# Kernel tuning notes

Hardware: AMD Instinct MI355X
Metric: run time of the kernel (lower is better)

The kernel has to match this reference:

```python
import jax, jax.numpy as jnp
import numpy as np

B = 100        # number of queries
N = 50000      # n_node
E = 600000     # n_edges
D = 128        # in_dim = out_dim (hidden_dim)
A = 64         # attn_dim
R = 200        # n_rel -> rela_embed has 2*R+1 = 401 rows


def setup_inputs() -> dict:
    key = jax.random.key(0)
    ks = jax.random.split(key, 14)
    q_sub = jax.random.randint(ks[0], (B,), 0, N)
    q_rel = jax.random.randint(ks[1], (B,), 0, 2 * R + 1)
    # edges: [E, 6]; col0=r_idx(<B), col2=rel(<2R+1), col4=sub(<N), col5=obj(<N); cols 1,3 unused
    c0 = jax.random.randint(ks[2], (E,), 0, B)
    c2 = jax.random.randint(ks[3], (E,), 0, 2 * R + 1)
    c4 = jax.random.randint(ks[4], (E,), 0, N)
    c5 = jax.random.randint(ks[5], (E,), 0, N)
    z = jnp.zeros((E,), dtype=jnp.int32)
    edges = jnp.stack([c0, z, c2, z, c4, c5], axis=1)
    hidden = jax.random.normal(ks[6], (N, D), dtype=jnp.float32)
    # learned parameters
    rela_embed = jax.random.normal(ks[7], (2 * R + 1, D), dtype=jnp.float32) * 0.02
    Ws = jax.random.normal(ks[8], (D, A), dtype=jnp.float32) * 0.05   # Ws_attn.weight^T
    Wr = jax.random.normal(ks[9], (D, A), dtype=jnp.float32) * 0.05   # Wr_attn.weight^T
    Wqr = jax.random.normal(ks[10], (D, A), dtype=jnp.float32) * 0.05 # Wqr_attn.weight^T
    bqr = jnp.zeros((A,), dtype=jnp.float32)
    wa = jax.random.normal(ks[11], (A, 1), dtype=jnp.float32) * 0.05  # w_alpha.weight^T
    ba = jnp.zeros((1,), dtype=jnp.float32)
    Wh = jax.random.normal(ks[12], (D, D), dtype=jnp.float32) * 0.05  # W_h.weight^T
    return {"q_sub": q_sub, "q_rel": q_rel, "hidden": hidden, "edges": edges,
            "n_node": N, "rela_embed": rela_embed, "Ws": Ws, "Wr": Wr,
            "Wqr": Wqr, "bqr": bqr, "wa": wa, "ba": ba, "Wh": Wh}


def reference(q_sub, q_rel, hidden, edges, n_node, rela_embed, Ws, Wr, Wqr, bqr, wa, ba, Wh):
    sub = edges[:, 4]
    rel = edges[:, 2]
    obj = edges[:, 5]
    r_idx = edges[:, 0]
    hs = hidden[sub]                       # [E, D] gather
    hr = rela_embed[rel]                   # [E, D] gather
    h_qr = rela_embed[q_rel][r_idx]        # [B, D] then gather -> [E, D]
    # attention score per edge
    pre = hs @ Ws + hr @ Wr + h_qr @ Wqr + bqr          # [E, A]
    alpha = jax.nn.sigmoid(jax.nn.relu(pre) @ wa + ba)   # [E, 1]
    message = alpha * (hs + hr)                          # [E, D]
    message_agg = jax.ops.segment_sum(message, obj, num_segments=n_node)  # [N, D]
    hidden_new = message_agg @ Wh                        # act = identity ('idd')
    return hidden_new
```

## Files before the change

### kernel.cpp

```cpp
#include <hip/hip_runtime.h>

#define DD 128
#define AA 64

static inline int idiv_up(int a, int b) { return (a + b - 1) / b; }

__global__ void rowmm_kernel(const float* __restrict__ src,
                             const float* __restrict__ W,
                             const float* __restrict__ bias,
                             const int* __restrict__ idx,
                             float* __restrict__ out, int nrows) {
    __shared__ float lds[4][DD];
    const int t = threadIdx.x;
    const int rl = t >> 6;
    const int a = t & 63;
    const int i = blockIdx.x * 4 + rl;
    if (i < nrows) {
        const int row = idx ? idx[i] : i;
        const float* srow = src + (long)row * DD;
        lds[rl][a]      = srow[a];
        lds[rl][a + 64] = srow[a + 64];
    }
    __syncthreads();
    if (i >= nrows) return;
    float acc = bias ? bias[a] : 0.0f;
    #pragma unroll 8
    for (int d = 0; d < DD; ++d)
        acc = fmaf(lds[rl][d], W[d * AA + a], acc);
    out[(long)i * AA + a] = acc;
}

__global__ void proj_gemm_kernel(const float* __restrict__ src,
                                 const float* __restrict__ W,
                                 float* __restrict__ out, int nrows) {
    __shared__ float lw[128 * 64];
    __shared__ float lht[128 * 64];
    const int t = threadIdx.x;
    const int rbase = blockIdx.x * 64;
    #pragma unroll
    for (int k = 0; k < 8192; k += 1024)
        *(float4*)&lw[k + t * 4] = *(const float4*)&W[k + t * 4];
    const int row = t & 63;
    const int d0 = (t >> 6) * 32;
    const int gr = rbase + row;
    #pragma unroll
    for (int j = 0; j < 8; ++j) {
        float4 v = make_float4(0.f, 0.f, 0.f, 0.f);
        if (gr < nrows) v = *(const float4*)&src[(long)gr * 128 + d0 + j * 4];
        lht[(d0 + j * 4 + 0) * 64 + row] = v.x;
        lht[(d0 + j * 4 + 1) * 64 + row] = v.y;
        lht[(d0 + j * 4 + 2) * 64 + row] = v.z;
        lht[(d0 + j * 4 + 3) * 64 + row] = v.w;
    }
    __syncthreads();
    const int r0 = (t & 15) * 4;
    const int c0 = (t >> 4) * 4;
    float acc[4][4] = {};
    #pragma unroll 4
    for (int d = 0; d < 128; ++d) {
        const float4 hv = *(const float4*)&lht[d * 64 + r0];
        const float4 wv = *(const float4*)&lw[d * 64 + c0];
        acc[0][0] = fmaf(hv.x, wv.x, acc[0][0]);
        acc[0][1] = fmaf(hv.x, wv.y, acc[0][1]);
        acc[0][2] = fmaf(hv.x, wv.z, acc[0][2]);
        acc[0][3] = fmaf(hv.x, wv.w, acc[0][3]);
        acc[1][0] = fmaf(hv.y, wv.x, acc[1][0]);
        acc[1][1] = fmaf(hv.y, wv.y, acc[1][1]);
        acc[1][2] = fmaf(hv.y, wv.z, acc[1][2]);
        acc[1][3] = fmaf(hv.y, wv.w, acc[1][3]);
        acc[2][0] = fmaf(hv.z, wv.x, acc[2][0]);
        acc[2][1] = fmaf(hv.z, wv.y, acc[2][1]);
        acc[2][2] = fmaf(hv.z, wv.z, acc[2][2]);
        acc[2][3] = fmaf(hv.z, wv.w, acc[2][3]);
        acc[3][0] = fmaf(hv.w, wv.x, acc[3][0]);
        acc[3][1] = fmaf(hv.w, wv.y, acc[3][1]);
        acc[3][2] = fmaf(hv.w, wv.z, acc[3][2]);
        acc[3][3] = fmaf(hv.w, wv.w, acc[3][3]);
    }
    #pragma unroll
    for (int i = 0; i < 4; ++i) {
        const int orow = rbase + r0 + i;
        if (orow < nrows)
            *(float4*)&out[(long)orow * 64 + c0] =
                make_float4(acc[i][0], acc[i][1], acc[i][2], acc[i][3]);
    }
}

__global__ void hist_kernel(const int* __restrict__ edges, int* deg, int E) {
    const int e = blockIdx.x * blockDim.x + threadIdx.x;
    if (e < E) atomicAdd(&deg[edges[(long)e * 6 + 5]], 1);
}

__global__ void scan1_kernel(const int* __restrict__ in, int* __restrict__ out,
                             int* __restrict__ bsum, int n) {
    __shared__ int tsum[256];
    const int t = threadIdx.x;
    const int base = blockIdx.x * 1024 + t * 4;
    int v[4];
    int s = 0;
    #pragma unroll
    for (int j = 0; j < 4; ++j) {
        v[j] = (base + j < n) ? in[base + j] : 0;
        s += v[j];
    }
    tsum[t] = s;
    __syncthreads();
    for (int o = 1; o < 256; o <<= 1) {
        int x = (t >= o) ? tsum[t - o] : 0;
        __syncthreads();
        tsum[t] += x;
        __syncthreads();
    }
    int run = (t > 0) ? tsum[t - 1] : 0;
    if (t == 255 && bsum) bsum[blockIdx.x] = tsum[255];
    #pragma unroll
    for (int j = 0; j < 4; ++j) {
        if (base + j < n) out[base + j] = run;
        run += v[j];
    }
}

__global__ void scan_add_kernel(int* offs, int* cur, const int* __restrict__ bsumx, int n) {
    const int i = blockIdx.x * blockDim.x + threadIdx.x;
    if (i < n) {
        const int v = offs[i] + bsumx[i >> 10];
        offs[i] = v;
        cur[i] = v;
    }
}

__global__ void scatter_kernel(const int* __restrict__ edges, int* cur,
                               int2* __restrict__ recs, int E) {
    const int e = blockIdx.x * blockDim.x + threadIdx.x;
    if (e >= E) return;
    const int* ed = edges + (long)e * 6;
    const int pos = atomicAdd(&cur[ed[5]], 1);
    recs[pos] = make_int2(ed[4], ed[2] | (ed[0] << 16));
}

__global__ void gather_kernel(const int2* __restrict__ recs,
                              const int* __restrict__ offs,
                              const float* __restrict__ hsWs,
                              const float* __restrict__ hrWr,
                              const float* __restrict__ hqrWqr,
                              const float* __restrict__ hidden,
                              const float* __restrict__ rela,
                              const float* __restrict__ wa,
                              const float* __restrict__ ba,
                              float* __restrict__ agg, int N, int E) {
    const int lane = threadIdx.x & 63;
    const int g = lane >> 4;
    const int l = lane & 15;
    const int v = (int)((blockIdx.x * blockDim.x + threadIdx.x) >> 6);
    if (v >= N) return;
    const float4 wav = *(const float4*)&wa[l * 4];
    const float bar = ba[0];
    const int start = offs[v];
    const int end = (v + 1 < N) ? offs[v + 1] : E;

    float4 acc0 = make_float4(0.f, 0.f, 0.f, 0.f);
    float4 acc1 = make_float4(0.f, 0.f, 0.f, 0.f);

    for (int base = start; base < end; base += 4) {
        const int k = base + g;
        const bool valid = (k < end);
        const int2 rec = valid ? recs[k] : make_int2(0, 0);
        const int sub  = rec.x;
        const int rel  = rec.y & 0xffff;
        const int ridx = rec.y >> 16;

        const float4 a4 = *(const float4*)&hsWs[sub * AA + l * 4];
        const float4 b4 = *(const float4*)&hrWr[rel * AA + l * 4];
        const float4 c4 = *(const float4*)&hqrWqr[ridx * AA + l * 4];
        float s = fmaxf(a4.x + b4.x + c4.x, 0.f) * wav.x;
        s = fmaf(fmaxf(a4.y + b4.y + c4.y, 0.f), wav.y, s);
        s = fmaf(fmaxf(a4.z + b4.z + c4.z, 0.f), wav.z, s);
        s = fmaf(fmaxf(a4.w + b4.w + c4.w, 0.f), wav.w, s);
        s += __shfl_xor(s, 1);
        s += __shfl_xor(s, 2);
        s += __shfl_xor(s, 4);
        s += __shfl_xor(s, 8);
        float alpha = __builtin_amdgcn_rcpf(1.0f + __expf(-(s + bar)));
        if (!valid) alpha = 0.0f;

        const float4 h0 = *(const float4*)&hidden[(long)sub * DD + l * 8];
        const float4 h1 = *(const float4*)&hidden[(long)sub * DD + l * 8 + 4];
        const float4 r0 = *(const float4*)&rela[rel * DD + l * 8];
        const float4 r1 = *(const float4*)&rela[rel * DD + l * 8 + 4];
        acc0.x = fmaf(alpha, h0.x + r0.x, acc0.x);
        acc0.y = fmaf(alpha, h0.y + r0.y, acc0.y);
        acc0.z = fmaf(alpha, h0.z + r0.z, acc0.z);
        acc0.w = fmaf(alpha, h0.w + r0.w, acc0.w);
        acc1.x = fmaf(alpha, h1.x + r1.x, acc1.x);
        acc1.y = fmaf(alpha, h1.y + r1.y, acc1.y);
        acc1.z = fmaf(alpha, h1.z + r1.z, acc1.z);
        acc1.w = fmaf(alpha, h1.w + r1.w, acc1.w);
    }

    #pragma unroll
    for (int o = 16; o <= 32; o <<= 1) {
        acc0.x += __shfl_xor(acc0.x, o);
        acc0.y += __shfl_xor(acc0.y, o);
        acc0.z += __shfl_xor(acc0.z, o);
        acc0.w += __shfl_xor(acc0.w, o);
        acc1.x += __shfl_xor(acc1.x, o);
        acc1.y += __shfl_xor(acc1.y, o);
        acc1.z += __shfl_xor(acc1.z, o);
        acc1.w += __shfl_xor(acc1.w, o);
    }
    if (g == 0) {
        *(float4*)&agg[(long)v * DD + l * 8]     = acc0;
        *(float4*)&agg[(long)v * DD + l * 8 + 4] = acc1;
    }
}

__global__ void out_gemm_kernel(const float* agg,
                                const float* __restrict__ Wh,
                                float* out, int nrows) {
    __shared__ float whs[64 * 128];
    __shared__ float ags[64 * 64];
    const int t = threadIdx.x;
    const int rbase = blockIdx.x * 64;
    const int j0 = (t & 31) * 4;
    const int rh = t >> 5;
    const int r0 = rh * 8;
    float acc[8][4];
    #pragma unroll
    for (int r = 0; r < 8; ++r)
        #pragma unroll
        for (int j = 0; j < 4; ++j) acc[r][j] = 0.0f;

    for (int dc = 0; dc < 128; dc += 64) {
        #pragma unroll
        for (int k = 0; k < 8192; k += 1024) {
            const int f = k + t * 4;
            *(float4*)&whs[f] = *(const float4*)&Wh[(long)dc * 128 + f];
        }
        #pragma unroll
        for (int k = 0; k < 4096; k += 1024) {
            const int f = k + t * 4;
            const int r = f >> 6;
            const int c = f & 63;
            float4 v = make_float4(0.0f, 0.0f, 0.0f, 0.0f);
            if (rbase + r < nrows)
                v = *(const float4*)&agg[(long)(rbase + r) * 128 + dc + c];
            *(float4*)&ags[f] = v;
        }
        __syncthreads();
        for (int d = 0; d < 64; d += 4) {
            const float4 wv0 = *(const float4*)&whs[(d + 0) * 128 + j0];
            const float4 wv1 = *(const float4*)&whs[(d + 1) * 128 + j0];
            const float4 wv2 = *(const float4*)&whs[(d + 2) * 128 + j0];
            const float4 wv3 = *(const float4*)&whs[(d + 3) * 128 + j0];
            #pragma unroll
            for (int r = 0; r < 8; ++r) {
                const float4 av = *(const float4*)&ags[(r0 + r) * 64 + d];
                acc[r][0] = fmaf(av.x, wv0.x, acc[r][0]);
                acc[r][1] = fmaf(av.x, wv0.y, acc[r][1]);
                acc[r][2] = fmaf(av.x, wv0.z, acc[r][2]);
                acc[r][3] = fmaf(av.x, wv0.w, acc[r][3]);
                acc[r][0] = fmaf(av.y, wv1.x, acc[r][0]);
                acc[r][1] = fmaf(av.y, wv1.y, acc[r][1]);
                acc[r][2] = fmaf(av.y, wv1.z, acc[r][2]);
                acc[r][3] = fmaf(av.y, wv1.w, acc[r][3]);
                acc[r][0] = fmaf(av.z, wv2.x, acc[r][0]);
                acc[r][1] = fmaf(av.z, wv2.y, acc[r][1]);
                acc[r][2] = fmaf(av.z, wv2.z, acc[r][2]);
                acc[r][3] = fmaf(av.z, wv2.w, acc[r][3]);
                acc[r][0] = fmaf(av.w, wv3.x, acc[r][0]);
                acc[r][1] = fmaf(av.w, wv3.y, acc[r][1]);
                acc[r][2] = fmaf(av.w, wv3.z, acc[r][2]);
                acc[r][3] = fmaf(av.w, wv3.w, acc[r][3]);
            }
        }
        __syncthreads();
    }
    #pragma unroll
    for (int r = 0; r < 8; ++r) {
        const int row = rbase + r0 + r;
        if (row < nrows)
            *(float4*)&out[(long)row * 128 + j0] =
                make_float4(acc[r][0], acc[r][1], acc[r][2], acc[r][3]);
    }
}

extern "C" void kernel_launch(void* const* d_in, const int* in_sizes, int n_in,
                              void* d_out, int out_size, void* d_ws, size_t ws_size,
                              hipStream_t stream) {
    const int*   q_rel  = (const int*)d_in[1];
    const float* hidden = (const float*)d_in[2];
    const int*   edges  = (const int*)d_in[3];
    const float* rela   = (const float*)d_in[5];
    const float* Ws     = (const float*)d_in[6];
    const float* Wr     = (const float*)d_in[7];
    const float* Wqr    = (const float*)d_in[8];
    const float* bqr    = (const float*)d_in[9];
    const float* wa     = (const float*)d_in[10];
    const float* ba     = (const float*)d_in[11];
    const float* Wh     = (const float*)d_in[12];

    const int B  = in_sizes[1];
    const int N  = in_sizes[2] / DD;
    const int E  = in_sizes[3] / 6;
    const int NR = in_sizes[5] / DD;

    float* out = (float*)d_out;

    float* hsWs   = (float*)d_ws;
    float* hrWr   = hsWs   + (size_t)N  * AA;
    float* hqrWqr = hrWr   + (size_t)NR * AA;
    int*   deg    = (int*)(hqrWqr + (size_t)B * AA);
    int*   cur    = deg  + N;
    int*   offs   = cur  + N;
    int*   bsum   = offs + N;
    int*   bsumx  = bsum + 64;
    int2*  recs   = (int2*)(bsumx + 64);

    const int nb = idiv_up(N, 1024);

    hipMemsetAsync(deg, 0, (size_t)N * sizeof(int), stream);
    proj_gemm_kernel<<<idiv_up(N, 64), 256, 0, stream>>>(hidden, Ws, hsWs, N);
    rowmm_kernel<<<idiv_up(NR, 4), 256, 0, stream>>>(rela, Wr, nullptr, nullptr, hrWr, NR);
    rowmm_kernel<<<idiv_up(B, 4), 256, 0, stream>>>(rela, Wqr, bqr, q_rel, hqrWqr, B);
    hist_kernel<<<idiv_up(E, 256), 256, 0, stream>>>(edges, deg, E);
    scan1_kernel<<<nb, 256, 0, stream>>>(deg, offs, bsum, N);
    scan1_kernel<<<1, 256, 0, stream>>>(bsum, bsumx, nullptr, nb);
    scan_add_kernel<<<idiv_up(N, 256), 256, 0, stream>>>(offs, cur, bsumx, N);
    scatter_kernel<<<idiv_up(E, 256), 256, 0, stream>>>(edges, cur, recs, E);
    gather_kernel<<<idiv_up(N * 64, 256), 256, 0, stream>>>(recs, offs, hsWs, hrWr, hqrWqr,
                                                            hidden, rela, wa, ba, out, N, E);
    out_gemm_kernel<<<idiv_up(N, 64), 256, 0, stream>>>(out, Wh, out, N);
}
```

Before: 306.1 us.

## Apply Wh before aggregation, merge projections into one kernel, store hsWs as bf16

Uses linearity to project hidden and rela_embed by Wh before the segment sum, so the gather accumulates already-transformed rows and the final out_gemm pass is dropped. All per-node and per-relation projections (Ws, Wr, Wqr, Wh) now run in one fused kernel launch. The hsWs attention term is stored as bf16 to halve its gather traffic. The trade-offs are an extra N×128 float intermediate written in the projection pass and reduced precision in the attention pre-activation.

After: 281.1 us. 1.09x faster.

```diff
diff --git a/kernel.cpp b/kernel.cpp
--- a/kernel.cpp
+++ b/kernel.cpp
@@ -5,84 +5,131 @@
 
 static inline int idiv_up(int a, int b) { return (a + b - 1) / b; }
 
-__global__ void rowmm_kernel(const float* __restrict__ src,
-                             const float* __restrict__ W,
-                             const float* __restrict__ bias,
-                             const int* __restrict__ idx,
-                             float* __restrict__ out, int nrows) {
-    __shared__ float lds[4][DD];
+__device__ __forceinline__ unsigned short f2bf(float f) {
+    unsigned u = __float_as_uint(f);
+    u += 0x7fff + ((u >> 16) & 1);
+    return (unsigned short)(u >> 16);
+}
+__device__ __forceinline__ float bf2f(unsigned short h) {
+    return __uint_as_float(((unsigned)h) << 16);
+}
+
+__global__ __launch_bounds__(256)
+void proj_all_kernel(const float* __restrict__ hidden,
+                     const float* __restrict__ rela,
+                     const int* __restrict__ q_rel,
+                     const float* __restrict__ Ws,
+                     const float* __restrict__ Wr,
+                     const float* __restrict__ Wqr,
+                     const float* __restrict__ bqr,
+                     const float* __restrict__ Wh,
+                     unsigned short* __restrict__ hsWs16,
+                     float* __restrict__ hiddenWh,
+                     float* __restrict__ hrWr,
+                     float* __restrict__ relaWh,
+                     float* __restrict__ hqrWqr,
+                     int N, int NR, int B, int nA, int nB) {
+    __shared__ float lht[128 * 64];
+    __shared__ float wbuf[128 * 64];
     const int t = threadIdx.x;
-    const int rl = t >> 6;
-    const int a = t & 63;
-    const int i = blockIdx.x * 4 + rl;
-    if (i < nrows) {
-        const int row = idx ? idx[i] : i;
-        const float* srow = src + (long)row * DD;
-        lds[rl][a]      = srow[a];
-        lds[rl][a + 64] = srow[a + 64];
-    }
-    __syncthreads();
-    if (i >= nrows) return;
-    float acc = bias ? bias[a] : 0.0f;
-    #pragma unroll 8
-    for (int d = 0; d < DD; ++d)
-        acc = fmaf(lds[rl][d], W[d * AA + a], acc);
-    out[(long)i * AA + a] = acc;
-}
-
-__global__ void proj_gemm_kernel(const float* __restrict__ src,
-                                 const float* __restrict__ W,
-                                 float* __restrict__ out, int nrows) {
-    __shared__ float lw[128 * 64];
-    __shared__ float lht[128 * 64];
-    const int t = threadIdx.x;
-    const int rbase = blockIdx.x * 64;
-    #pragma unroll
-    for (int k = 0; k < 8192; k += 1024)
-        *(float4*)&lw[k + t * 4] = *(const float4*)&W[k + t * 4];
+    const int bid = blockIdx.x;
+    int type, rbase, nrows;
+    const float* src;
+    if (bid < nA)           { type = 0; rbase = bid * 64;             nrows = N;  src = hidden; }
+    else if (bid < nA + nB) { type = 1; rbase = (bid - nA) * 64;      nrows = NR; src = rela; }
+    else                    { type = 2; rbase = (bid - nA - nB) * 64; nrows = B;  src = rela; }
+
     const int row = t & 63;
     const int d0 = (t >> 6) * 32;
     const int gr = rbase + row;
+    const float* srow = nullptr;
+    if (gr < nrows) {
+        const int sr = (type == 2) ? q_rel[gr] : gr;
+        srow = src + (long)sr * DD;
+    }
     #pragma unroll
     for (int j = 0; j < 8; ++j) {
         float4 v = make_float4(0.f, 0.f, 0.f, 0.f);
-        if (gr < nrows) v = *(const float4*)&src[(long)gr * 128 + d0 + j * 4];
+        if (srow) v = *(const float4*)&srow[d0 + j * 4];
         lht[(d0 + j * 4 + 0) * 64 + row] = v.x;
         lht[(d0 + j * 4 + 1) * 64 + row] = v.y;
         lht[(d0 + j * 4 + 2) * 64 + row] = v.z;
         lht[(d0 + j * 4 + 3) * 64 + row] = v.w;
     }
-    __syncthreads();
+
     const int r0 = (t & 15) * 4;
     const int c0 = (t >> 4) * 4;
-    float acc[4][4] = {};
-    #pragma unroll 4
-    for (int d = 0; d < 128; ++d) {
-        const float4 hv = *(const float4*)&lht[d * 64 + r0];
-        const float4 wv = *(const float4*)&lw[d * 64 + c0];
-        acc[0][0] = fmaf(hv.x, wv.x, acc[0][0]);
-        acc[0][1] = fmaf(hv.x, wv.y, acc[0][1]);
-        acc[0][2] = fmaf(hv.x, wv.z, acc[0][2]);
-        acc[0][3] = fmaf(hv.x, wv.w, acc[0][3]);
-        acc[1][0] = fmaf(hv.y, wv.x, acc[1][0]);
-        acc[1][1] = fmaf(hv.y, wv.y, acc[1][1]);
-        acc[1][2] = fmaf(hv.y, wv.z, acc[1][2]);
-        acc[1][3] = fmaf(hv.y, wv.w, acc[1][3]);
-        acc[2][0] = fmaf(hv.z, wv.x, acc[2][0]);
-        acc[2][1] = fmaf(hv.z, wv.y, acc[2][1]);
-        acc[2][2] = fmaf(hv.z, wv.z, acc[2][2]);
-        acc[2][3] = fmaf(hv.z, wv.w, acc[2][3]);
-        acc[3][0] = fmaf(hv.w, wv.x, acc[3][0]);
-        acc[3][1] = fmaf(hv.w, wv.y, acc[3][1]);
-        acc[3][2] = fmaf(hv.w, wv.z, acc[3][2]);
-        acc[3][3] = fmaf(hv.w, wv.w, acc[3][3]);
-    }
-    #pragma unroll
-    for (int i = 0; i < 4; ++i) {
-        const int orow = rbase + r0 + i;
-        if (orow < nrows)
-            *(float4*)&out[(long)orow * 64 + c0] =
-                make_float4(acc[i][0], acc[i][1], acc[i][2], acc[i][3]);
+    const int nph = (type == 2) ? 1 : 3;
+
+    for (int p = 0; p < nph; ++p) {
+        const float* W;
+        int ldw, off;
+        if (p == 0) {
+            W = (type == 0) ? Ws : (type == 1) ? Wr : Wqr;
+            ldw = 64; off = 0;
+        } else {
+            W = Wh; ldw = 128; off = (p - 1) * 64;
+        }
+        #pragma unroll
+        for (int k = 0; k < 8192; k += 1024) {
+            const int f = k + t * 4;
+            *(float4*)&wbuf[f] = *(const float4*)&W[(long)(f >> 6) * ldw + off + (f & 63)];
+        }
+        __syncthreads();
+
+        float acc[4][4] = {};
+        #pragma unroll 4
+        for (int d = 0; d < 128; ++d) {
+            const float4 hv = *(const float4*)&lht[d * 64 + r0];
+            const float4 wv = *(const float4*)&wbuf[d * 64 + c0];
+            acc[0][0] = fmaf(hv.x, wv.x, acc[0][0]);
+            acc[0][1] = fmaf(hv.x, wv.y, acc[0][1]);
+            acc[0][2] = fmaf(hv.x, wv.z, acc[0][2]);
+            acc[0][3] = fmaf(hv.x, wv.w, acc[0][3]);
+            acc[1][0] = fmaf(hv.y, wv.x, acc[1][0]);
+            acc[1][1] = fmaf(hv.y, wv.y, acc[1][1]);
+            acc[1][2] = fmaf(hv.y, wv.z, acc[1][2]);
+            acc[1][3] = fmaf(hv.y, wv.w, acc[1][3]);
+            acc[2][0] = fmaf(hv.z, wv.x, acc[2][0]);
+            acc[2][1] = fmaf(hv.z, wv.y, acc[2][1]);
+            acc[2][2] = fmaf(hv.z, wv.z, acc[2][2]);
+            acc[2][3] = fmaf(hv.z, wv.w, acc[2][3]);
+            acc[3][0] = fmaf(hv.w, wv.x, acc[3][0]);
+            acc[3][1] = fmaf(hv.w, wv.y, acc[3][1]);
+            acc[3][2] = fmaf(hv.w, wv.z, acc[3][2]);
+            acc[3][3] = fmaf(hv.w, wv.w, acc[3][3]);
+        }
+
+        #pragma unroll
+        for (int i = 0; i < 4; ++i) {
+            const int orow = rbase + r0 + i;
+            if (orow >= nrows) continue;
+            if (type == 0) {
+                if (p == 0) {
+                    ushort4 o;
+                    o.x = f2bf(acc[i][0]); o.y = f2bf(acc[i][1]);
+                    o.z = f2bf(acc[i][2]); o.w = f2bf(acc[i][3]);
+                    *(ushort4*)&hsWs16[(long)orow * 64 + c0] = o;
+                } else {
+                    *(float4*)&hiddenWh[(long)orow * 128 + off + c0] =
+                        make_float4(acc[i][0], acc[i][1], acc[i][2], acc[i][3]);
+                }
+            } else if (type == 1) {
+                if (p == 0) {
+                    *(float4*)&hrWr[(long)orow * 64 + c0] =
+                        make_float4(acc[i][0], acc[i][1], acc[i][2], acc[i][3]);
+                } else {
+                    *(float4*)&relaWh[(long)orow * 128 + off + c0] =
+                        make_float4(acc[i][0], acc[i][1], acc[i][2], acc[i][3]);
+                }
+            } else {
+                const float4 bq = *(const float4*)&bqr[c0];
+                *(float4*)&hqrWqr[(long)orow * 64 + c0] =
+                    make_float4(acc[i][0] + bq.x, acc[i][1] + bq.y,
+                                acc[i][2] + bq.z, acc[i][3] + bq.w);
+            }
+        }
+        __syncthreads();
     }
 }
 
@@ -138,16 +185,17 @@
     recs[pos] = make_int2(ed[4], ed[2] | (ed[0] << 16));
 }
 
-__global__ void gather_kernel(const int2* __restrict__ recs,
-                              const int* __restrict__ offs,
-                              const float* __restrict__ hsWs,
-                              const float* __restrict__ hrWr,
-                              const float* __restrict__ hqrWqr,
-                              const float* __restrict__ hidden,
-                              const float* __restrict__ rela,
-                              const float* __restrict__ wa,
-                              const float* __restrict__ ba,
-                              float* __restrict__ agg, int N, int E) {
+__global__ __launch_bounds__(256)
+void gather_kernel(const int2* __restrict__ recs,
+                   const int* __restrict__ offs,
+                   const unsigned short* __restrict__ hsWs16,
+                   const float* __restrict__ hrWr,
+                   const float* __restrict__ hqrWqr,
+                   const float* __restrict__ hiddenWh,
+                   const float* __restrict__ relaWh,
+                   const float* __restrict__ wa,
+                   const float* __restrict__ ba,
+                   float* __restrict__ out, int N, int E) {
     const int lane = threadIdx.x & 63;
     const int g = lane >> 4;
     const int l = lane & 15;
@@ -169,13 +217,13 @@
         const int rel  = rec.y & 0xffff;
         const int ridx = rec.y >> 16;
 
-        const float4 a4 = *(const float4*)&hsWs[sub * AA + l * 4];
+        const ushort4 hw = *(const ushort4*)&hsWs16[(long)sub * AA + l * 4];
         const float4 b4 = *(const float4*)&hrWr[rel * AA + l * 4];
         const float4 c4 = *(const float4*)&hqrWqr[ridx * AA + l * 4];
-        float s = fmaxf(a4.x + b4.x + c4.x, 0.f) * wav.x;
-        s = fmaf(fmaxf(a4.y + b4.y + c4.y, 0.f), wav.y, s);
-        s = fmaf(fmaxf(a4.z + b4.z + c4.z, 0.f), wav.z, s);
-        s = fmaf(fmaxf(a4.w + b4.w + c4.w, 0.f), wav.w, s);
+        float s = fmaxf(bf2f(hw.x) + b4.x + c4.x, 0.f) * wav.x;
+        s = fmaf(fmaxf(bf2f(hw.y) + b4.y + c4.y, 0.f), wav.y, s);
+        s = fmaf(fmaxf(bf2f(hw.z) + b4.z + c4.z, 0.f), wav.z, s);
+        s = fmaf(fmaxf(bf2f(hw.w) + b4.w + c4.w, 0.f), wav.w, s);
         s += __shfl_xor(s, 1);
         s += __shfl_xor(s, 2);
         s += __shfl_xor(s, 4);
@@ -183,10 +231,10 @@
         float alpha = __builtin_amdgcn_rcpf(1.0f + __expf(-(s + bar)));
         if (!valid) alpha = 0.0f;
 
-        const float4 h0 = *(const float4*)&hidden[(long)sub * DD + l * 8];
-        const float4 h1 = *(const float4*)&hidden[(long)sub * DD + l * 8 + 4];
-        const float4 r0 = *(const float4*)&rela[rel * DD + l * 8];
-        const float4 r1 = *(const float4*)&rela[rel * DD + l * 8 + 4];
+        const float4 h0 = *(const float4*)&hiddenWh[(long)sub * DD + l * 8];
+        const float4 h1 = *(const float4*)&hiddenWh[(long)sub * DD + l * 8 + 4];
+        const float4 r0 = *(const float4*)&relaWh[rel * DD + l * 8];
+        const float4 r1 = *(const float4*)&relaWh[rel * DD + l * 8 + 4];
         acc0.x = fmaf(alpha, h0.x + r0.x, acc0.x);
         acc0.y = fmaf(alpha, h0.y + r0.y, acc0.y);
         acc0.z = fmaf(alpha, h0.z + r0.z, acc0.z);
@@ -209,78 +257,8 @@
         acc1.w += __shfl_xor(acc1.w, o);
     }
     if (g == 0) {
-        *(float4*)&agg[(long)v * DD + l * 8]     = acc0;
-        *(float4*)&agg[(long)v * DD + l * 8 + 4] = acc1;
-    }
-}
-
-__global__ void out_gemm_kernel(const float* agg,
-                                const float* __restrict__ Wh,
-                                float* out, int nrows) {
-    __shared__ float whs[64 * 128];
-    __shared__ float ags[64 * 64];
-    const int t = threadIdx.x;
-    const int rbase = blockIdx.x * 64;
-    const int j0 = (t & 31) * 4;
-    const int rh = t >> 5;
-    const int r0 = rh * 8;
-    float acc[8][4];
-    #pragma unroll
-    for (int r = 0; r < 8; ++r)
-        #pragma unroll
-        for (int j = 0; j < 4; ++j) acc[r][j] = 0.0f;
-
-    for (int dc = 0; dc < 128; dc += 64) {
-        #pragma unroll
-        for (int k = 0; k < 8192; k += 1024) {
-            const int f = k + t * 4;
-            *(float4*)&whs[f] = *(const float4*)&Wh[(long)dc * 128 + f];
-        }
-        #pragma unroll
-        for (int k = 0; k < 4096; k += 1024) {
-            const int f = k + t * 4;
-            const int r = f >> 6;
-            const int c = f & 63;
-            float4 v = make_float4(0.0f, 0.0f, 0.0f, 0.0f);
-            if (rbase + r < nrows)
-                v = *(const float4*)&agg[(long)(rbase + r) * 128 + dc + c];
-            *(float4*)&ags[f] = v;
-        }
-        __syncthreads();
-        for (int d = 0; d < 64; d += 4) {
-            const float4 wv0 = *(const float4*)&whs[(d + 0) * 128 + j0];
-            const float4 wv1 = *(const float4*)&whs[(d + 1) * 128 + j0];
-            const float4 wv2 = *(const float4*)&whs[(d + 2) * 128 + j0];
-            const float4 wv3 = *(const float4*)&whs[(d + 3) * 128 + j0];
-            #pragma unroll
-            for (int r = 0; r < 8; ++r) {
-                const float4 av = *(const float4*)&ags[(r0 + r) * 64 + d];
-                acc[r][0] = fmaf(av.x, wv0.x, acc[r][0]);
-                acc[r][1] = fmaf(av.x, wv0.y, acc[r][1]);
-                acc[r][2] = fmaf(av.x, wv0.z, acc[r][2]);
-                acc[r][3] = fmaf(av.x, wv0.w, acc[r][3]);
-                acc[r][0] = fmaf(av.y, wv1.x, acc[r][0]);
-                acc[r][1] = fmaf(av.y, wv1.y, acc[r][1]);
-                acc[r][2] = fmaf(av.y, wv1.z, acc[r][2]);
-                acc[r][3] = fmaf(av.y, wv1.w, acc[r][3]);
-                acc[r][0] = fmaf(av.z, wv2.x, acc[r][0]);
-                acc[r][1] = fmaf(av.z, wv2.y, acc[r][1]);
-                acc[r][2] = fmaf(av.z, wv2.z, acc[r][2]);
-                acc[r][3] = fmaf(av.z, wv2.w, acc[r][3]);
-                acc[r][0] = fmaf(av.w, wv3.x, acc[r][0]);
-                acc[r][1] = fmaf(av.w, wv3.y, acc[r][1]);
-                acc[r][2] = fmaf(av.w, wv3.z, acc[r][2]);
-                acc[r][3] = fmaf(av.w, wv3.w, acc[r][3]);
-            }
-        }
-        __syncthreads();
-    }
-    #pragma unroll
-    for (int r = 0; r < 8; ++r) {
-        const int row = rbase + r0 + r;
-        if (row < nrows)
-            *(float4*)&out[(long)row * 128 + j0] =
-                make_float4(acc[r][0], acc[r][1], acc[r][2], acc[r][3]);
+        *(float4*)&out[(long)v * DD + l * 8]     = acc0;
+        *(float4*)&out[(long)v * DD + l * 8 + 4] = acc1;
     }
 }
 
@@ -306,28 +284,32 @@
 
     float* out = (float*)d_out;
 
-    float* hsWs   = (float*)d_ws;
-    float* hrWr   = hsWs   + (size_t)N  * AA;
-    float* hqrWqr = hrWr   + (size_t)NR * AA;
-    int*   deg    = (int*)(hqrWqr + (size_t)B * AA);
-    int*   cur    = deg  + N;
-    int*   offs   = cur  + N;
-    int*   bsum   = offs + N;
-    int*   bsumx  = bsum + 64;
-    int2*  recs   = (int2*)(bsumx + 64);
-
+    unsigned short* hsWs16 = (unsigned short*)d_ws;
+    float* hiddenWh = (float*)(hsWs16 + (size_t)N * AA);
+    float* hrWr     = hiddenWh + (size_t)N * DD;
+    float* relaWh   = hrWr + (size_t)NR * AA;
+    float* hqrWqr   = relaWh + (size_t)NR * DD;
+    int*   deg      = (int*)(hqrWqr + (size_t)B * AA);
+    int*   cur      = deg  + N;
+    int*   offs     = cur  + N;
+    int*   bsum     = offs + N;
+    int*   bsumx    = bsum + 64;
+    int2*  recs     = (int2*)(bsumx + 64);
+
+    const int nA = idiv_up(N, 64);
+    const int nB = idiv_up(NR, 64);
+    const int nC = idiv_up(B, 64);
     const int nb = idiv_up(N, 1024);
 
     hipMemsetAsync(deg, 0, (size_t)N * sizeof(int), stream);
-    proj_gemm_kernel<<<idiv_up(N, 64), 256, 0, stream>>>(hidden, Ws, hsWs, N);
-    rowmm_kernel<<<idiv_up(NR, 4), 256, 0, stream>>>(rela, Wr, nullptr, nullptr, hrWr, NR);
-    rowmm_kernel<<<idiv_up(B, 4), 256, 0, stream>>>(rela, Wqr, bqr, q_rel, hqrWqr, B);
+    proj_all_kernel<<<nA + nB + nC, 256, 0, stream>>>(
+        hidden, rela, q_rel, Ws, Wr, Wqr, bqr, Wh,
+        hsWs16, hiddenWh, hrWr, relaWh, hqrWqr, N, NR, B, nA, nB);
     hist_kernel<<<idiv_up(E, 256), 256, 0, stream>>>(edges, deg, E);
     scan1_kernel<<<nb, 256, 0, stream>>>(deg, offs, bsum, N);
     scan1_kernel<<<1, 256, 0, stream>>>(bsum, bsumx, nullptr, nb);
     scan_add_kernel<<<idiv_up(N, 256), 256, 0, stream>>>(offs, cur, bsumx, N);
     scatter_kernel<<<idiv_up(E, 256), 256, 0, stream>>>(edges, cur, recs, E);
-    gather_kernel<<<idiv_up(N * 64, 256), 256, 0, stream>>>(recs, offs, hsWs, hrWr, hqrWqr,
-                                                            hidden, rela, wa, ba, out, N, E);
-    out_gemm_kernel<<<idiv_up(N, 64), 256, 0, stream>>>(out, Wh, out, N);
-}
+    gather_kernel<<<idiv_up(N * 64, 256), 256, 0, stream>>>(
+        recs, offs, hsWs16, hrWr, hqrWqr, hiddenWh, relaWh, wa, ba, out, N, E);
+}
```
